# Kernel optimization log

Measured on AMD Instinct MI355X. Metric: run time of the kernel, lower is better.

## Reference

```python
import jax, jax.numpy as jnp
import numpy as np

B, N, H = 8, 128, 512   # batch, num_sent (n == m required by the 'all' branch), hidden_size
D = 2 * H               # bi-LSTM output dim
SCALE = 0.05


def setup_inputs() -> dict:
    key = jax.random.key(0)
    ks = jax.random.split(key, 24)
    p = lambda k, shape: (jax.random.normal(k, shape, dtype=jnp.float32) * SCALE)
    return {
        "x0_enc": jax.random.normal(ks[0], (B, N, D), dtype=jnp.float32),
        "x1_enc": jax.random.normal(ks[1], (B, N, D), dtype=jnp.float32),
        # concat_attention
        "Wc1": p(ks[2], (D, H)), "Wc2": p(ks[3], (D, H)), "vc": p(ks[4], (H,)),
        # bilinear_attention
        "Wb": p(ks[5], (D, D)),
        # dot_attention x2 (separate params)
        "Wd1": p(ks[6], (D, H)), "vd1": p(ks[7], (H,)),
        "Wd2": p(ks[8], (D, H)), "vd2": p(ks[9], (H,)),
        # minus_attention (Ws/vs are unused in forward)
        "Wm": p(ks[10], (D, H)), "vm": p(ks[11], (H,)),
        # aggregation_layer
        "Wq": p(ks[12], (D, H)), "vq": p(ks[13], (H,)),
        "Wp1": p(ks[14], (2 * D, H)), "Wp2": p(ks[15], (D, H)), "vp": p(ks[16], (H,)),
        "Wpred": p(ks[17], (2 * D, 2)), "bpred": jnp.zeros((2,), dtype=jnp.float32),
    }


def _dot_att(x, y, Wd, vd):
    # sjt[b,m,n] = vd . tanh(Wd(x[b,n] * y[b,m]))  -- pairwise elementwise product + MLP
    z = jnp.tanh(jnp.einsum("bnd,bmd,dh->bmnh", x, y, Wd))  # [B,m,n,H]
    s = jnp.einsum("bmnh,h->bmn", z, vd)
    a = jax.nn.softmax(s, axis=2)
    return jnp.einsum("bmn,bnd->bmd", a, x)


def _minus_att(x, y, Wm, vm):
    # Wm is linear, so Wm(x_n - y_m) = (x@Wm)_n - (y@Wm)_m
    a, b = x @ Wm, y @ Wm                                    # [B,n,H], [B,m,H]
    z = jnp.tanh(a[:, None, :, :] - b[:, :, None, :])        # [B,m,n,H]
    s = jnp.einsum("bmnh,h->bmn", z, vm)
    att = jax.nn.softmax(s, axis=2)
    return jnp.einsum("bmn,bnd->bmd", att, x)


def _concat_att(x, y, Wc1, Wc2, vc):
    a, b = x @ Wc1, y @ Wc2                                  # [B,n,H], [B,m,H]
    z = jnp.tanh(a[:, None, :, :] + b[:, :, None, :])        # [B,m,n,H]
    s = jnp.einsum("bmnh,h->bmn", z, vc)
    att = jax.nn.softmax(s, axis=2)
    return jnp.einsum("bmn,bnd->bmd", att, x)


def _bilinear_att(x, y, Wb):
    s = jnp.einsum("bmd,bnd->bmn", y, x @ Wb)
    att = jax.nn.softmax(s, axis=2)
    return jnp.einsum("bmn,bnd->bmd", att, x)


def reference(x0_enc, x1_enc, Wc1, Wc2, vc, Wb, Wd1, vd1, Wd2, vd2, Wm, vm,
              Wq, vq, Wp1, Wp2, vp, Wpred, bpred):
    x0, x1 = x0_enc, x1_enc
    # attention_fx('all')
    qtc = _concat_att(x0, x1, Wc1, Wc2, vc)
    qtb = _bilinear_att(x0, x1, Wb)
    qts = _dot_att(x0, x1, Wd1, vd1)
    qtd = _dot_att(x1, x0, Wd2, vd2)
    qtm = _minus_att(x0, x1, Wm, vm)
    agg_res = jnp.max(jnp.stack([x1, qts, qtc, qtd, qtb, qtm], axis=0), axis=0)  # [B,m,2H]
    # MultiAtt: dropout is identity in eval
    agg_rep = jnp.concatenate([x1, agg_res], axis=2)                             # [B,m,4H]
    # aggregation_layer
    sj = jnp.einsum("bnh,h->bn", jnp.tanh(x0 @ Wq), vq)
    rq = jnp.einsum("bn,bnd->bd", jax.nn.softmax(sj, axis=1), x0)                # [B,2H]
    t = agg_rep @ Wp1 + (rq @ Wp2)[:, None, :]                                   # [B,m,H]
    sp = jax.nn.softmax(jnp.einsum("bmh,h->bm", t, vp), axis=1)
    rp = jnp.einsum("bm,bmd->bd", sp, agg_rep)                                   # [B,4H]
    out = jax.nn.relu(rp @ Wpred + bpred)                                        # [B,2]
    return out
```

## Files before the change

kernel.cpp:

```cpp
#include <hip/hip_runtime.h>
#include <hip/hip_bf16.h>

static constexpr int Bc = 8, Nc = 128, Dc = 1024, Hc = 512;
static constexpr int BM = Bc * Nc;

typedef _Float16 half8 __attribute__((ext_vector_type(8)));
typedef __fp16 fp16x2 __attribute__((ext_vector_type(2)));
typedef float floatx4 __attribute__((ext_vector_type(4)));

__device__ __forceinline__ float fast_tanh(float x) {
  x = fminf(fmaxf(x, -15.f), 15.f);
  float e = __expf(2.f * x);
  return (e - 1.f) / (e + 1.f);
}

__device__ __forceinline__ unsigned pkh2(float a, float b) {
  fp16x2 h = __builtin_amdgcn_cvt_pkrtz(a, b);
  return __builtin_bit_cast(unsigned, h);
}

__device__ __forceinline__ ushort f2h(float f) {
  _Float16 h = (_Float16)f;
  return __builtin_bit_cast(ushort, h);
}

__device__ __forceinline__ float block_sum256(float v, float* buf4) {
  #pragma unroll
  for (int o = 32; o; o >>= 1) v += __shfl_down(v, o, 64);
  const int w = threadIdx.x >> 6, lane = threadIdx.x & 63;
  if (lane == 0) buf4[w] = v;
  __syncthreads();
  return buf4[0] + buf4[1] + buf4[2] + buf4[3];
}

__global__ __launch_bounds__(256) void cvt_both(const float* __restrict__ x0,
                                                const float* __restrict__ x1,
                                                ushort* __restrict__ o0,
                                                ushort* __restrict__ o1) {
  int bi = blockIdx.x;
  const float* src = (bi < 512) ? x0 : x1;
  ushort* dst = (bi < 512) ? o0 : o1;
  int off = (bi & 511);
  int i = (off * 256 + threadIdx.x) * 8;
  float4 a = *reinterpret_cast<const float4*>(&src[i]);
  float4 b = *reinterpret_cast<const float4*>(&src[i + 4]);
  uint4 o;
  o.x = pkh2(a.x, a.y); o.y = pkh2(a.z, a.w);
  o.z = pkh2(b.x, b.y); o.w = pkh2(b.z, b.w);
  *reinterpret_cast<uint4*>(&dst[i]) = o;
}

struct TJobs {
  const float* src[7];
  ushort* dst[7];
  int J[7];
};
__global__ __launch_bounds__(256) void conv_transpose_multi(TJobs jobs) {
  const int job = blockIdx.z;
  const int J = jobs.J[job];
  const int h0 = blockIdx.y * 64;
  if (h0 >= J) return;
  const float* W = jobs.src[job];
  ushort* WT = jobs.dst[job];
  __shared__ float tile[64][65];
  const int d0 = blockIdx.x * 64;
  const int tid = threadIdx.x;
  #pragma unroll
  for (int i = 0; i < 16; i++) {
    int idx = tid + i * 256;
    int dd = idx >> 6, hh = idx & 63;
    tile[dd][hh] = W[(size_t)(d0 + dd) * J + h0 + hh];
  }
  __syncthreads();
  #pragma unroll
  for (int i = 0; i < 16; i++) {
    int idx = tid + i * 256;
    int hh = idx >> 6, dd = idx & 63;
    WT[(size_t)(h0 + hh) * Dc + d0 + dd] = f2h(tile[dd][hh]);
  }
}

__global__ __launch_bounds__(256) void gemm_bt(const ushort* __restrict__ A,
                                               const ushort* __restrict__ BT,
                                               float* __restrict__ Cf,
                                               ushort* __restrict__ Ch,
                                               int K, int ldc,
                                               size_t sA, size_t sB, size_t sC) {
  const int bz = blockIdx.z;
  A  += (size_t)bz * sA;
  BT += (size_t)bz * sB;
  const int m0 = blockIdx.y * 64, n0 = blockIdx.x * 64;
  __shared__ __align__(16) ushort Asl[64][40];
  __shared__ __align__(16) ushort Bsl[64][40];
  const int tid = threadIdx.x, wave = tid >> 6, lane = tid & 63;
  const int quad = lane >> 4, l15 = lane & 15;
  const int wr = (wave & 1) * 32, wc = (wave >> 1) * 32;
  const int rSt = tid >> 2, kSt8 = (tid & 3) * 8;
  floatx4 acc[2][2];
  #pragma unroll
  for (int i = 0; i < 2; i++)
    #pragma unroll
    for (int j = 0; j < 2; j++) acc[i][j] = (floatx4){0.f, 0.f, 0.f, 0.f};
  uint4 pa = *reinterpret_cast<const uint4*>(&A[(size_t)(m0 + rSt) * K + kSt8]);
  uint4 pb = *reinterpret_cast<const uint4*>(&BT[(size_t)(n0 + rSt) * K + kSt8]);
  for (int k0 = 0; k0 < K; k0 += 32) {
    *reinterpret_cast<uint4*>(&Asl[rSt][kSt8]) = pa;
    *reinterpret_cast<uint4*>(&Bsl[rSt][kSt8]) = pb;
    __syncthreads();
    if (k0 + 32 < K) {
      pa = *reinterpret_cast<const uint4*>(&A[(size_t)(m0 + rSt) * K + k0 + 32 + kSt8]);
      pb = *reinterpret_cast<const uint4*>(&BT[(size_t)(n0 + rSt) * K + k0 + 32 + kSt8]);
    }
    half8 af[2], bb[2];
    #pragma unroll
    for (int i = 0; i < 2; i++)
      af[i] = *reinterpret_cast<const half8*>(&Asl[wr + i * 16 + l15][quad * 8]);
    #pragma unroll
    for (int j = 0; j < 2; j++)
      bb[j] = *reinterpret_cast<const half8*>(&Bsl[wc + j * 16 + l15][quad * 8]);
    #pragma unroll
    for (int i = 0; i < 2; i++)
      #pragma unroll
      for (int j = 0; j < 2; j++)
        acc[i][j] = __builtin_amdgcn_mfma_f32_16x16x32_f16(af[i], bb[j], acc[i][j], 0, 0, 0);
    __syncthreads();
  }
  if (Ch) {
    #pragma unroll
    for (int i = 0; i < 2; i++)
      #pragma unroll
      for (int j = 0; j < 2; j++)
        #pragma unroll
        for (int r = 0; r < 4; r++) {
          int row = m0 + wr + i * 16 + quad * 4 + r;
          int col = n0 + wc + j * 16 + l15;
          Ch[(size_t)bz * sC + (size_t)row * ldc + col] = f2h(acc[i][j][r]);
        }
  } else {
    #pragma unroll
    for (int i = 0; i < 2; i++)
      #pragma unroll
      for (int j = 0; j < 2; j++)
        #pragma unroll
        for (int r = 0; r < 4; r++) {
          int row = m0 + wr + i * 16 + quad * 4 + r;
          int col = n0 + wc + j * 16 + l15;
          Cf[(size_t)bz * sC + (size_t)row * ldc + col] = acc[i][j][r];
        }
  }
}

__global__ __launch_bounds__(512, 2) void dot_scores_mfma8(const ushort* __restrict__ X0h,
                                                           const ushort* __restrict__ X1h,
                                                           const ushort* __restrict__ WdT1,
                                                           const ushort* __restrict__ WdT2,
                                                           const float* __restrict__ vd1,
                                                           const float* __restrict__ vd2,
                                                           float* __restrict__ Sd) {
  const int which = blockIdx.z;
  const ushort* Xh = which ? X1h : X0h;
  const ushort* Yh = which ? X0h : X1h;
  const ushort* WdT = which ? WdT2 : WdT1;
  const float* v = which ? vd2 : vd1;
  float* S = Sd + (size_t)which * (BM * Nc);

  const int mp = blockIdx.y;
  const int b = mp >> 6;
  const int hBase = blockIdx.x * 256;
  const int tid = threadIdx.x;
  const int wave = tid >> 6, lane = tid & 63;
  const int quad = lane >> 4, l15 = lane & 15;
  const int mg = wave >> 2, wn = (wave >> 1) & 1, wh = wave & 1;

  __shared__ __align__(16) char smraw[53248];
  ushort* As0 = (ushort*)smraw;
  ushort* As1 = (ushort*)(smraw + 8192);
  ushort* Bs0 = (ushort*)(smraw + 16384);
  ushort* Bs1 = (ushort*)(smraw + 32768);
  ushort* ylh = (ushort*)(smraw + 49152);
  float (*red)[33] = (float(*)[33])smraw;

  {
    const uint* Y0 = (const uint*)(Yh + (size_t)(mp * 2) * Dc);
    uint* dst = (uint*)ylh;
    dst[tid] = Y0[tid];
    dst[tid + 512] = Y0[tid + 512];
  }

  floatx4 acc[4][8];
  #pragma unroll
  for (int i = 0; i < 4; i++)
    #pragma unroll
    for (int j = 0; j < 8; j++) acc[i][j] = (floatx4){0.f, 0.f, 0.f, 0.f};

  const ushort* Xb = Xh + (size_t)b * Nc * Dc;
  const int nA = tid >> 2;
  const int ch8 = (tid & 3) * 8;

  half8 xv;
  uint4 bv0, bv1;
  auto loads = [&](int s) {
    xv = *reinterpret_cast<const half8*>(Xb + (size_t)nA * Dc + s * 32 + ch8);
    const ushort* wp = WdT + (size_t)(hBase + nA) * Dc + s * 32 + ch8;
    bv0 = *reinterpret_cast<const uint4*>(wp);
    bv1 = *reinterpret_cast<const uint4*>(wp + 128 * Dc);
  };
  auto stage = [&](ushort* Asb, ushort* Bsb) {
    *reinterpret_cast<half8*>(Asb + (size_t)nA * 32 + ch8) = xv;
    *reinterpret_cast<uint4*>(Bsb + (size_t)nA * 32 + ch8) = bv0;
    *reinterpret_cast<uint4*>(Bsb + 4096 + (size_t)nA * 32 + ch8) = bv1;
  };
  auto mfma_step = [&](int s, const ushort* Asb, const ushort* Bsb) {
    half8 yv = *reinterpret_cast<const half8*>(ylh + mg * 1024 + s * 32 + quad * 8);
    half8 af[4], bfr[8];
    #pragma unroll
    for (int i = 0; i < 4; i++) {
      half8 xf = *reinterpret_cast<const half8*>(Asb + (wn * 64 + i * 16 + l15) * 32 + quad * 8);
      af[i] = xf * yv;
    }
    #pragma unroll
    for (int j = 0; j < 8; j++)
      bfr[j] = *reinterpret_cast<const half8*>(Bsb + (wh * 128 + j * 16 + l15) * 32 + quad * 8);
    #pragma unroll
    for (int i = 0; i < 4; i++)
      #pragma unroll
      for (int j = 0; j < 8; j++)
        acc[i][j] = __builtin_amdgcn_mfma_f32_16x16x32_f16(af[i], bfr[j], acc[i][j], 0, 0, 0);
  };

  loads(0);
  stage(As0, Bs0);
  loads(1);
  __syncthreads();
  #pragma unroll 1
  for (int s = 0; s < 32; s++) {
    if (s + 1 < 32) {
      stage((s + 1) & 1 ? As1 : As0, (s + 1) & 1 ? Bs1 : Bs0);
      if (s + 2 < 32) loads(s + 2);
    }
    mfma_step(s, s & 1 ? As1 : As0, s & 1 ? Bs1 : Bs0);
    __syncthreads();
  }

  float vv[8];
  #pragma unroll
  for (int j = 0; j < 8; j++) vv[j] = v[hBase + wh * 128 + j * 16 + l15];
  #pragma unroll
  for (int i = 0; i < 4; i++)
    #pragma unroll
    for (int r = 0; r < 4; r++) {
      float p = 0.f;
      #pragma unroll
      for (int j = 0; j < 8; j++) p = fmaf(vv[j], fast_tanh(acc[i][j][r]), p);
      red[mg * 128 + wn * 64 + i * 16 + quad * 4 + r][wh * 16 + l15] = p;
    }
  __syncthreads();
  if (tid < 256) {
    float s = 0.f;
    #pragma unroll
    for (int c = 0; c < 32; c++) s += red[tid][c];
    atomicAdd(&S[(size_t)mp * 256 + tid], s);
  }
}

__global__ __launch_bounds__(256) void addtanh_tiled2(const float* __restrict__ C1,
                                                      const float* __restrict__ C2,
                                                      const float* __restrict__ vc,
                                                      const float* __restrict__ vm,
                                                      float* __restrict__ Sc,
                                                      float* __restrict__ Sm) {
  const int nt = blockIdx.x, mt = blockIdx.y;
  const int which = blockIdx.z >> 3, b = blockIdx.z & 7;
  const float* Arow = C1 + which * 512;
  const float* Brow = C2 + which * 512;
  const float* v = which ? vm : vc;
  const float sign = which ? -1.f : 1.f;
  float* S = which ? Sm : Sc;
  __shared__ __align__(16) float at[16][516];
  __shared__ __align__(16) float bt2[16][516];
  __shared__ __align__(16) float vl[512];
  const int tid = threadIdx.x;
  #pragma unroll
  for (int p = 0; p < 8; p++) {
    int idx = p * 256 + tid;
    int r = idx >> 7, c4 = (idx & 127) * 4;
    *reinterpret_cast<float4*>(&at[r][c4]) =
        *reinterpret_cast<const float4*>(&Arow[(size_t)(b * Nc + nt * 16 + r) * 1024 + c4]);
    *reinterpret_cast<float4*>(&bt2[r][c4]) =
        *reinterpret_cast<const float4*>(&Brow[(size_t)(b * Nc + mt * 16 + r) * 1024 + c4]);
  }
  if (tid < 128)
    *reinterpret_cast<float4*>(&vl[tid * 4]) = *reinterpret_cast<const float4*>(&v[tid * 4]);
  __syncthreads();
  const int m = tid >> 4, n = tid & 15;
  float acc = 0.f;
  #pragma unroll 4
  for (int c = 0; c < 512; c += 4) {
    float4 av = *reinterpret_cast<const float4*>(&at[n][c]);
    float4 bv = *reinterpret_cast<const float4*>(&bt2[m][c]);
    float4 vv = *reinterpret_cast<const float4*>(&vl[c]);
    acc = fmaf(vv.x, fast_tanh(fmaf(sign, bv.x, av.x)), acc);
    acc = fmaf(vv.y, fast_tanh(fmaf(sign, bv.y, av.y)), acc);
    acc = fmaf(vv.z, fast_tanh(fmaf(sign, bv.z, av.z)), acc);
    acc = fmaf(vv.w, fast_tanh(fmaf(sign, bv.w, av.w)), acc);
  }
  S[(size_t)(b * Nc + mt * 16 + m) * Nc + nt * 16 + n] = acc;
}

__global__ __launch_bounds__(128) void softmax128(float* __restrict__ S) {
  const int row = blockIdx.x;
  const int tid = threadIdx.x;
  float x = S[(size_t)row * 128 + tid];
  __shared__ float mbuf[2], sbuf[2];
  float mx = x;
  #pragma unroll
  for (int o = 32; o; o >>= 1) mx = fmaxf(mx, __shfl_down(mx, o, 64));
  if ((tid & 63) == 0) mbuf[tid >> 6] = mx;
  __syncthreads();
  mx = fmaxf(mbuf[0], mbuf[1]);
  float e = __expf(x - mx);
  float sm = e;
  #pragma unroll
  for (int o = 32; o; o >>= 1) sm += __shfl_down(sm, o, 64);
  if ((tid & 63) == 0) sbuf[tid >> 6] = sm;
  __syncthreads();
  sm = sbuf[0] + sbuf[1];
  S[(size_t)row * 128 + tid] = e / sm;
}

#define FMA4(acc, s, v)                  \
  acc.x = fmaf(s, v.x, acc.x);           \
  acc.y = fmaf(s, v.y, acc.y);           \
  acc.z = fmaf(s, v.z, acc.z);           \
  acc.w = fmaf(s, v.w, acc.w)

__global__ __launch_bounds__(256) void agg_max(const float* __restrict__ x0,
                                               const float* __restrict__ x1,
                                               const float* __restrict__ Sc,
                                               const float* __restrict__ Sb,
                                               const float* __restrict__ Sd1,
                                               const float* __restrict__ Sd2,
                                               const float* __restrict__ Sm,
                                               const float* __restrict__ u,
                                               float* __restrict__ agg,
                                               float* __restrict__ score) {
  const int bm = blockIdx.x;
  const int b = bm >> 7;
  const int tid = threadIdx.x;
  __shared__ float w[5][128];
  if (tid < 128) {
    w[0][tid] = Sc[(size_t)bm * Nc + tid];
    w[1][tid] = Sb[(size_t)bm * Nc + tid];
    w[2][tid] = Sd1[(size_t)bm * Nc + tid];
    w[3][tid] = Sd2[(size_t)bm * Nc + tid];
    w[4][tid] = Sm[(size_t)bm * Nc + tid];
  }
  __syncthreads();
  const int d0 = tid * 4;
  float4 qc = {0, 0, 0, 0}, qb = {0, 0, 0, 0}, qs = {0, 0, 0, 0};
  float4 qd = {0, 0, 0, 0}, qm = {0, 0, 0, 0};
  const float* X0b = x0 + (size_t)b * Nc * Dc;
  const float* X1b = x1 + (size_t)b * Nc * Dc;
  for (int n = 0; n < Nc; n++) {
    float4 xv = *reinterpret_cast<const float4*>(&X0b[(size_t)n * Dc + d0]);
    float4 yv = *reinterpret_cast<const float4*>(&X1b[(size_t)n * Dc + d0]);
    float wc = w[0][n], wb = w[1][n], ws = w[2][n], wd = w[3][n], wm = w[4][n];
    FMA4(qc, wc, xv);
    FMA4(qb, wb, xv);
    FMA4(qs, ws, xv);
    FMA4(qd, wd, yv);
    FMA4(qm, wm, xv);
  }
  float4 x1v = *reinterpret_cast<const float4*>(&x1[(size_t)bm * Dc + d0]);
  float4 r;
  r.x = fmaxf(x1v.x, fmaxf(fmaxf(qs.x, qc.x), fmaxf(fmaxf(qd.x, qb.x), qm.x)));
  r.y = fmaxf(x1v.y, fmaxf(fmaxf(qs.y, qc.y), fmaxf(fmaxf(qd.y, qb.y), qm.y)));
  r.z = fmaxf(x1v.z, fmaxf(fmaxf(qs.z, qc.z), fmaxf(fmaxf(qd.z, qb.z), qm.z)));
  r.w = fmaxf(x1v.w, fmaxf(fmaxf(qs.w, qc.w), fmaxf(fmaxf(qd.w, qb.w), qm.w)));
  *reinterpret_cast<float4*>(&agg[(size_t)bm * Dc + d0]) = r;
  float4 u1 = *reinterpret_cast<const float4*>(&u[d0]);
  float4 u2 = *reinterpret_cast<const float4*>(&u[Dc + d0]);
  float p = x1v.x * u1.x + x1v.y * u1.y + x1v.z * u1.z + x1v.w * u1.w +
            r.x * u2.x + r.y * u2.y + r.z * u2.z + r.w * u2.w;
  __shared__ float buf4[4];
  p = block_sum256(p, buf4);
  if (tid == 0) score[bm] = p;
}

__global__ __launch_bounds__(64) void compute_u(const float* __restrict__ Wp1,
                                                const float* __restrict__ vp,
                                                float* __restrict__ u) {
  const int d2 = blockIdx.x;
  const int tid = threadIdx.x;
  float p = 0.f;
  #pragma unroll
  for (int h = tid; h < Hc; h += 64) p = fmaf(Wp1[(size_t)d2 * Hc + h], vp[h], p);
  #pragma unroll
  for (int o = 32; o; o >>= 1) p += __shfl_down(p, o, 64);
  if (tid == 0) u[d2] = p;
}

__global__ __launch_bounds__(256) void final_out(const float* __restrict__ x1,
                                                 const float* __restrict__ agg,
                                                 const float* __restrict__ score,
                                                 const float* __restrict__ Wpred,
                                                 const float* __restrict__ bpred,
                                                 float* __restrict__ out) {
  const int b = blockIdx.x;
  const int tid = threadIdx.x;
  __shared__ float spL[128];
  __shared__ float mbuf[2], sbuf[2];
  if (tid < 128) {
    float x = score[b * Nc + tid];
    float mx = x;
    #pragma unroll
    for (int o = 32; o; o >>= 1) mx = fmaxf(mx, __shfl_down(mx, o, 64));
    if ((tid & 63) == 0) mbuf[tid >> 6] = mx;
  }
  __syncthreads();
  if (tid < 128) {
    float x = score[b * Nc + tid];
    float mx = fmaxf(mbuf[0], mbuf[1]);
    float e = __expf(x - mx);
    float sm = e;
    #pragma unroll
    for (int o = 32; o; o >>= 1) sm += __shfl_down(sm, o, 64);
    if ((tid & 63) == 0) sbuf[tid >> 6] = sm;
    spL[tid] = e;
  }
  __syncthreads();
  const float inv = 1.f / (sbuf[0] + sbuf[1]);
  const int d2 = tid * 8;
  float w0[8], w1[8];
  #pragma unroll
  for (int i = 0; i < 8; i++) {
    w0[i] = Wpred[(size_t)(d2 + i) * 2 + 0];
    w1[i] = Wpred[(size_t)(d2 + i) * 2 + 1];
  }
  const float* src = (d2 < Dc) ? (x1 + (size_t)b * Nc * Dc + d2)
                               : (agg + (size_t)b * Nc * Dc + (d2 - Dc));
  float p0 = 0.f, p1 = 0.f;
  for (int m = 0; m < Nc; m++) {
    float s = spL[m] * inv;
    const float* r = src + (size_t)m * Dc;
    #pragma unroll
    for (int i = 0; i < 8; i++) {
      float sc = s * r[i];
      p0 = fmaf(sc, w0[i], p0);
      p1 = fmaf(sc, w1[i], p1);
    }
  }
  #pragma unroll
  for (int o = 32; o; o >>= 1) {
    p0 += __shfl_down(p0, o, 64);
    p1 += __shfl_down(p1, o, 64);
  }
  __shared__ float r0[4], r1[4];
  const int w = tid >> 6, lane = tid & 63;
  if (lane == 0) { r0[w] = p0; r1[w] = p1; }
  __syncthreads();
  if (tid == 0) {
    float q0 = r0[0] + r0[1] + r0[2] + r0[3] + bpred[0];
    float q1 = r1[0] + r1[1] + r1[2] + r1[3] + bpred[1];
    out[b * 2 + 0] = fmaxf(q0, 0.f);
    out[b * 2 + 1] = fmaxf(q1, 0.f);
  }
}

extern "C" void kernel_launch(void* const* d_in, const int* in_sizes, int n_in,
                              void* d_out, int out_size, void* d_ws, size_t ws_size,
                              hipStream_t stream) {
  const float* x0    = (const float*)d_in[0];
  const float* x1    = (const float*)d_in[1];
  const float* Wc1   = (const float*)d_in[2];
  const float* Wc2   = (const float*)d_in[3];
  const float* vc    = (const float*)d_in[4];
  const float* Wb    = (const float*)d_in[5];
  const float* Wd1   = (const float*)d_in[6];
  const float* vd1   = (const float*)d_in[7];
  const float* Wd2   = (const float*)d_in[8];
  const float* vd2   = (const float*)d_in[9];
  const float* Wm    = (const float*)d_in[10];
  const float* vm    = (const float*)d_in[11];
  const float* Wp1   = (const float*)d_in[14];
  const float* vp    = (const float*)d_in[16];
  const float* Wpred = (const float*)d_in[17];
  const float* bpred = (const float*)d_in[18];
  float* out = (float*)d_out;

  float* ws = (float*)d_ws;
  float* C1     = ws;
  float* C2     = C1 + 1048576;
  float* sc     = C2 + 1048576;
  float* sb     = sc + 131072;
  float* sd1    = sb + 131072;
  float* sd2    = sd1 + 131072;
  float* smv    = sd2 + 131072;
  float* u      = smv + 131072;
  float* score2 = u + 2048;
  ushort* x0h   = (ushort*)(score2 + 1024);
  ushort* x1h   = x0h + 1048576;
  ushort* W1T   = x1h + 1048576;
  ushort* W2T   = W1T + 1048576;
  ushort* WbT   = W2T + 1048576;
  ushort* xWbh  = WbT + 1048576;
  ushort* wdT1  = xWbh + 1048576;
  ushort* wdT2  = wdT1 + 524288;
  float* agg    = C1;

  cvt_both<<<1024, 256, 0, stream>>>(x0, x1, x0h, x1h);
  TJobs tj;
  tj.src[0] = Wd1; tj.dst[0] = wdT1;            tj.J[0] = Hc;
  tj.src[1] = Wd2; tj.dst[1] = wdT2;            tj.J[1] = Hc;
  tj.src[2] = Wc1; tj.dst[2] = W1T;             tj.J[2] = Hc;
  tj.src[3] = Wm;  tj.dst[3] = W1T + 512 * Dc;  tj.J[3] = Hc;
  tj.src[4] = Wc2; tj.dst[4] = W2T;             tj.J[4] = Hc;
  tj.src[5] = Wm;  tj.dst[5] = W2T + 512 * Dc;  tj.J[5] = Hc;
  tj.src[6] = Wb;  tj.dst[6] = WbT;             tj.J[6] = Dc;
  conv_transpose_multi<<<dim3(16, 16, 7), 256, 0, stream>>>(tj);
  compute_u<<<2 * Dc, 64, 0, stream>>>(Wp1, vp, u);

  gemm_bt<<<dim3(16, 16, 1), 256, 0, stream>>>(x0h, W1T, C1, nullptr, Dc, 1024, 0, 0, 0);
  gemm_bt<<<dim3(16, 16, 1), 256, 0, stream>>>(x1h, W2T, C2, nullptr, Dc, 1024, 0, 0, 0);
  gemm_bt<<<dim3(16, 16, 1), 256, 0, stream>>>(x0h, WbT, nullptr, xWbh, Dc, 1024, 0, 0, 0);
  gemm_bt<<<dim3(2, 2, 8), 256, 0, stream>>>(x1h, xWbh, sb, nullptr, Dc, 128,
                                             131072, 131072, 16384);

  addtanh_tiled2<<<dim3(8, 8, 16), 256, 0, stream>>>(C1, C2, vc, vm, sc, smv);

  (void)hipMemsetAsync(sd1, 0, 2 * 131072 * sizeof(float), stream);
  dot_scores_mfma8<<<dim3(2, BM / 2, 2), 512, 0, stream>>>(x0h, x1h, wdT1, wdT2, vd1, vd2, sd1);

  softmax128<<<5 * BM, 128, 0, stream>>>(sc);

  agg_max<<<BM, 256, 0, stream>>>(x0, x1, sc, sb, sd1, sd2, smv, u, agg, score2);

  final_out<<<Bc, 256, 0, stream>>>(x1, agg, score2, Wpred, bpred, out);
}
```

Baseline: 624.3 us.

## Batch projection GEMMs, fuse softmax into agg_max, read Wd fragments from global

Merges the three projection GEMM launches into one gemm_proj kernel that picks its job from blockIdx.z. Removes the separate softmax128 pass by computing the five row softmaxes inside agg_max, which saves a kernel launch and a read/write of the score arrays. In the dot-score kernel, the Wd B-fragments are loaded straight from global memory instead of being staged in LDS. This cuts shared memory use, which may raise occupancy, but every MFMA step now depends on uncoalesced global loads that mostly hit in cache.

Measured after the change: 842.7 us. 1.35x slower.

```diff
diff --git a/kernel.cpp b/kernel.cpp
--- a/kernel.cpp
+++ b/kernel.cpp
@@ -80,10 +80,83 @@
   }
 }
 
+struct GJobs {
+  const ushort* A[3];
+  const ushort* BT[3];
+  float* Cf[3];
+  ushort* Ch[3];
+};
+__global__ __launch_bounds__(256) void gemm_proj(GJobs g) {
+  const int job = blockIdx.z;
+  const ushort* A = g.A[job];
+  const ushort* BT = g.BT[job];
+  float* Cf = g.Cf[job];
+  ushort* Ch = g.Ch[job];
+  const int K = Dc, ldc = 1024;
+  const int m0 = blockIdx.y * 64, n0 = blockIdx.x * 64;
+  __shared__ __align__(16) ushort Asl[64][40];
+  __shared__ __align__(16) ushort Bsl[64][40];
+  const int tid = threadIdx.x, wave = tid >> 6, lane = tid & 63;
+  const int quad = lane >> 4, l15 = lane & 15;
+  const int wr = (wave & 1) * 32, wc = (wave >> 1) * 32;
+  const int rSt = tid >> 2, kSt8 = (tid & 3) * 8;
+  floatx4 acc[2][2];
+  #pragma unroll
+  for (int i = 0; i < 2; i++)
+    #pragma unroll
+    for (int j = 0; j < 2; j++) acc[i][j] = (floatx4){0.f, 0.f, 0.f, 0.f};
+  uint4 pa = *reinterpret_cast<const uint4*>(&A[(size_t)(m0 + rSt) * K + kSt8]);
+  uint4 pb = *reinterpret_cast<const uint4*>(&BT[(size_t)(n0 + rSt) * K + kSt8]);
+  for (int k0 = 0; k0 < K; k0 += 32) {
+    *reinterpret_cast<uint4*>(&Asl[rSt][kSt8]) = pa;
+    *reinterpret_cast<uint4*>(&Bsl[rSt][kSt8]) = pb;
+    __syncthreads();
+    if (k0 + 32 < K) {
+      pa = *reinterpret_cast<const uint4*>(&A[(size_t)(m0 + rSt) * K + k0 + 32 + kSt8]);
+      pb = *reinterpret_cast<const uint4*>(&BT[(size_t)(n0 + rSt) * K + k0 + 32 + kSt8]);
+    }
+    half8 af[2], bb[2];
+    #pragma unroll
+    for (int i = 0; i < 2; i++)
+      af[i] = *reinterpret_cast<const half8*>(&Asl[wr + i * 16 + l15][quad * 8]);
+    #pragma unroll
+    for (int j = 0; j < 2; j++)
+      bb[j] = *reinterpret_cast<const half8*>(&Bsl[wc + j * 16 + l15][quad * 8]);
+    #pragma unroll
+    for (int i = 0; i < 2; i++)
+      #pragma unroll
+      for (int j = 0; j < 2; j++)
+        acc[i][j] = __builtin_amdgcn_mfma_f32_16x16x32_f16(af[i], bb[j], acc[i][j], 0, 0, 0);
+    __syncthreads();
+  }
+  if (Ch) {
+    #pragma unroll
+    for (int i = 0; i < 2; i++)
+      #pragma unroll
+      for (int j = 0; j < 2; j++)
+        #pragma unroll
+        for (int r = 0; r < 4; r++) {
+          int row = m0 + wr + i * 16 + quad * 4 + r;
+          int col = n0 + wc + j * 16 + l15;
+          Ch[(size_t)row * ldc + col] = f2h(acc[i][j][r]);
+        }
+  } else {
+    #pragma unroll
+    for (int i = 0; i < 2; i++)
+      #pragma unroll
+      for (int j = 0; j < 2; j++)
+        #pragma unroll
+        for (int r = 0; r < 4; r++) {
+          int row = m0 + wr + i * 16 + quad * 4 + r;
+          int col = n0 + wc + j * 16 + l15;
+          Cf[(size_t)row * ldc + col] = acc[i][j][r];
+        }
+  }
+}
+
 __global__ __launch_bounds__(256) void gemm_bt(const ushort* __restrict__ A,
                                                const ushort* __restrict__ BT,
                                                float* __restrict__ Cf,
-                                               ushort* __restrict__ Ch,
                                                int K, int ldc,
                                                size_t sA, size_t sB, size_t sC) {
   const int bz = blockIdx.z;
@@ -125,32 +198,19 @@
         acc[i][j] = __builtin_amdgcn_mfma_f32_16x16x32_f16(af[i], bb[j], acc[i][j], 0, 0, 0);
     __syncthreads();
   }
-  if (Ch) {
-    #pragma unroll
-    for (int i = 0; i < 2; i++)
-      #pragma unroll
-      for (int j = 0; j < 2; j++)
-        #pragma unroll
-        for (int r = 0; r < 4; r++) {
-          int row = m0 + wr + i * 16 + quad * 4 + r;
-          int col = n0 + wc + j * 16 + l15;
-          Ch[(size_t)bz * sC + (size_t)row * ldc + col] = f2h(acc[i][j][r]);
-        }
-  } else {
-    #pragma unroll
-    for (int i = 0; i < 2; i++)
-      #pragma unroll
-      for (int j = 0; j < 2; j++)
-        #pragma unroll
-        for (int r = 0; r < 4; r++) {
-          int row = m0 + wr + i * 16 + quad * 4 + r;
-          int col = n0 + wc + j * 16 + l15;
-          Cf[(size_t)bz * sC + (size_t)row * ldc + col] = acc[i][j][r];
-        }
-  }
-}
-
-__global__ __launch_bounds__(512, 2) void dot_scores_mfma8(const ushort* __restrict__ X0h,
+  #pragma unroll
+  for (int i = 0; i < 2; i++)
+    #pragma unroll
+    for (int j = 0; j < 2; j++)
+      #pragma unroll
+      for (int r = 0; r < 4; r++) {
+        int row = m0 + wr + i * 16 + quad * 4 + r;
+        int col = n0 + wc + j * 16 + l15;
+        Cf[(size_t)bz * sC + (size_t)row * ldc + col] = acc[i][j][r];
+      }
+}
+
+__global__ __launch_bounds__(512, 2) void dot_scores_mfma9(const ushort* __restrict__ X0h,
                                                            const ushort* __restrict__ X1h,
                                                            const ushort* __restrict__ WdT1,
                                                            const ushort* __restrict__ WdT2,
@@ -172,12 +232,10 @@
   const int quad = lane >> 4, l15 = lane & 15;
   const int mg = wave >> 2, wn = (wave >> 1) & 1, wh = wave & 1;
 
-  __shared__ __align__(16) char smraw[53248];
+  __shared__ __align__(16) char smraw[33792];
   ushort* As0 = (ushort*)smraw;
   ushort* As1 = (ushort*)(smraw + 8192);
-  ushort* Bs0 = (ushort*)(smraw + 16384);
-  ushort* Bs1 = (ushort*)(smraw + 32768);
-  ushort* ylh = (ushort*)(smraw + 49152);
+  ushort* ylh = (ushort*)(smraw + 16384);
   float (*red)[33] = (float(*)[33])smraw;
 
   {
@@ -197,20 +255,16 @@
   const int nA = tid >> 2;
   const int ch8 = (tid & 3) * 8;
 
+  const ushort* Wb_ = WdT + (size_t)(hBase + wh * 128 + l15) * Dc + quad * 8;
+
   half8 xv;
-  uint4 bv0, bv1;
-  auto loads = [&](int s) {
+  auto loadx = [&](int s) {
     xv = *reinterpret_cast<const half8*>(Xb + (size_t)nA * Dc + s * 32 + ch8);
-    const ushort* wp = WdT + (size_t)(hBase + nA) * Dc + s * 32 + ch8;
-    bv0 = *reinterpret_cast<const uint4*>(wp);
-    bv1 = *reinterpret_cast<const uint4*>(wp + 128 * Dc);
   };
-  auto stage = [&](ushort* Asb, ushort* Bsb) {
+  auto stage = [&](ushort* Asb) {
     *reinterpret_cast<half8*>(Asb + (size_t)nA * 32 + ch8) = xv;
-    *reinterpret_cast<uint4*>(Bsb + (size_t)nA * 32 + ch8) = bv0;
-    *reinterpret_cast<uint4*>(Bsb + 4096 + (size_t)nA * 32 + ch8) = bv1;
   };
-  auto mfma_step = [&](int s, const ushort* Asb, const ushort* Bsb) {
+  auto mfma_step = [&](int s, const ushort* Asb) {
     half8 yv = *reinterpret_cast<const half8*>(ylh + mg * 1024 + s * 32 + quad * 8);
     half8 af[4], bfr[8];
     #pragma unroll
@@ -220,7 +274,7 @@
     }
     #pragma unroll
     for (int j = 0; j < 8; j++)
-      bfr[j] = *reinterpret_cast<const half8*>(Bsb + (wh * 128 + j * 16 + l15) * 32 + quad * 8);
+      bfr[j] = *reinterpret_cast<const half8*>(Wb_ + (size_t)(j * 16) * Dc + s * 32);
     #pragma unroll
     for (int i = 0; i < 4; i++)
       #pragma unroll
@@ -228,17 +282,17 @@
         acc[i][j] = __builtin_amdgcn_mfma_f32_16x16x32_f16(af[i], bfr[j], acc[i][j], 0, 0, 0);
   };
 
-  loads(0);
-  stage(As0, Bs0);
-  loads(1);
+  loadx(0);
+  stage(As0);
+  loadx(1);
   __syncthreads();
   #pragma unroll 1
   for (int s = 0; s < 32; s++) {
     if (s + 1 < 32) {
-      stage((s + 1) & 1 ? As1 : As0, (s + 1) & 1 ? Bs1 : Bs0);
-      if (s + 2 < 32) loads(s + 2);
+      stage((s + 1) & 1 ? As1 : As0);
+      if (s + 2 < 32) loadx(s + 2);
     }
-    mfma_step(s, s & 1 ? As1 : As0, s & 1 ? Bs1 : Bs0);
+    mfma_step(s, s & 1 ? As1 : As0);
     __syncthreads();
   }
 
@@ -307,27 +361,6 @@
   S[(size_t)(b * Nc + mt * 16 + m) * Nc + nt * 16 + n] = acc;
 }
 
-__global__ __launch_bounds__(128) void softmax128(float* __restrict__ S) {
-  const int row = blockIdx.x;
-  const int tid = threadIdx.x;
-  float x = S[(size_t)row * 128 + tid];
-  __shared__ float mbuf[2], sbuf[2];
-  float mx = x;
-  #pragma unroll
-  for (int o = 32; o; o >>= 1) mx = fmaxf(mx, __shfl_down(mx, o, 64));
-  if ((tid & 63) == 0) mbuf[tid >> 6] = mx;
-  __syncthreads();
-  mx = fmaxf(mbuf[0], mbuf[1]);
-  float e = __expf(x - mx);
-  float sm = e;
-  #pragma unroll
-  for (int o = 32; o; o >>= 1) sm += __shfl_down(sm, o, 64);
-  if ((tid & 63) == 0) sbuf[tid >> 6] = sm;
-  __syncthreads();
-  sm = sbuf[0] + sbuf[1];
-  S[(size_t)row * 128 + tid] = e / sm;
-}
-
 #define FMA4(acc, s, v)                  \
   acc.x = fmaf(s, v.x, acc.x);           \
   acc.y = fmaf(s, v.y, acc.y);           \
@@ -348,6 +381,7 @@
   const int b = bm >> 7;
   const int tid = threadIdx.x;
   __shared__ float w[5][128];
+  __shared__ float sred[4];
   if (tid < 128) {
     w[0][tid] = Sc[(size_t)bm * Nc + tid];
     w[1][tid] = Sb[(size_t)bm * Nc + tid];
@@ -356,6 +390,25 @@
     w[4][tid] = Sm[(size_t)bm * Nc + tid];
   }
   __syncthreads();
+  for (int r = 0; r < 5; r++) {
+    float x = (tid < 128) ? w[r][tid] : -3.0e38f;
+    float mx = x;
+    #pragma unroll
+    for (int o = 32; o; o >>= 1) mx = fmaxf(mx, __shfl_down(mx, o, 64));
+    if ((tid & 63) == 0) sred[tid >> 6] = mx;
+    __syncthreads();
+    float M = fmaxf(sred[0], sred[1]);
+    float e = (tid < 128) ? __expf(x - M) : 0.f;
+    float sm = e;
+    #pragma unroll
+    for (int o = 32; o; o >>= 1) sm += __shfl_down(sm, o, 64);
+    __syncthreads();
+    if ((tid & 63) == 0) sred[tid >> 6] = sm;
+    __syncthreads();
+    float inv = 1.f / (sred[0] + sred[1]);
+    if (tid < 128) w[r][tid] = e * inv;
+    __syncthreads();
+  }
   const int d0 = tid * 4;
   float4 qc = {0, 0, 0, 0}, qb = {0, 0, 0, 0}, qs = {0, 0, 0, 0};
   float4 qd = {0, 0, 0, 0}, qm = {0, 0, 0, 0};
@@ -520,18 +573,18 @@
   conv_transpose_multi<<<dim3(16, 16, 7), 256, 0, stream>>>(tj);
   compute_u<<<2 * Dc, 64, 0, stream>>>(Wp1, vp, u);
 
-  gemm_bt<<<dim3(16, 16, 1), 256, 0, stream>>>(x0h, W1T, C1, nullptr, Dc, 1024, 0, 0, 0);
-  gemm_bt<<<dim3(16, 16, 1), 256, 0, stream>>>(x1h, W2T, C2, nullptr, Dc, 1024, 0, 0, 0);
-  gemm_bt<<<dim3(16, 16, 1), 256, 0, stream>>>(x0h, WbT, nullptr, xWbh, Dc, 1024, 0, 0, 0);
-  gemm_bt<<<dim3(2, 2, 8), 256, 0, stream>>>(x1h, xWbh, sb, nullptr, Dc, 128,
+  GJobs gj;
+  gj.A[0] = x0h; gj.BT[0] = W1T; gj.Cf[0] = C1; gj.Ch[0] = nullptr;
+  gj.A[1] = x1h; gj.BT[1] = W2T; gj.Cf[1] = C2; gj.Ch[1] = nullptr;
+  gj.A[2] = x0h; gj.BT[2] = WbT; gj.Cf[2] = nullptr; gj.Ch[2] = xWbh;
+  gemm_proj<<<dim3(16, 16, 3), 256, 0, stream>>>(gj);
+  gemm_bt<<<dim3(2, 2, 8), 256, 0, stream>>>(x1h, xWbh, sb, Dc, 128,
                                              131072, 131072, 16384);
 
   addtanh_tiled2<<<dim3(8, 8, 16), 256, 0, stream>>>(C1, C2, vc, vm, sc, smv);
 
   (void)hipMemsetAsync(sd1, 0, 2 * 131072 * sizeof(float), stream);
-  dot_scores_mfma8<<<dim3(2, BM / 2, 2), 512, 0, stream>>>(x0h, x1h, wdT1, wdT2, vd1, vd2, sd1);
-
-  softmax128<<<5 * BM, 128, 0, stream>>>(sc);
+  dot_scores_mfma9<<<dim3(2, BM / 2, 2), 512, 0, stream>>>(x0h, x1h, wdT1, wdT2, vd1, vd2, sd1);
 
   agg_max<<<BM, 256, 0, stream>>>(x0, x1, sc, sb, sd1, sd2, smv, u, agg, score2);
 
```
